# Kernel optimization log

Hardware: AMD Instinct MI355X
Metric: run time of the kernel (lower is better)

The kernel has to match this reference:

```python
import math
import jax, jax.numpy as jnp
import numpy as np

C = 32        # per-head dim
N_HEAD = 8
C_IN = 128

def setup_inputs() -> dict:
    key = jax.random.key(0)
    ks = jax.random.split(key, 10)
    B, S = 1, 256
    sc = 0.05  # keep logits in a sane range
    x    = jax.random.normal(ks[0], (B, S, S, C_IN), dtype=jnp.float32)
    bias = jax.random.normal(ks[1], (B, N_HEAD, S, S), dtype=jnp.float32)
    attention_mask = jax.random.randint(ks[2], (B, S, S), 0, 2).astype(bool)
    Wq = jax.random.normal(ks[3], (C_IN, C * N_HEAD), dtype=jnp.float32) * sc
    Wk = jax.random.normal(ks[4], (C_IN, C * N_HEAD), dtype=jnp.float32) * sc
    Wv = jax.random.normal(ks[5], (C_IN, C * N_HEAD), dtype=jnp.float32) * sc
    Wo = jax.random.normal(ks[6], (C * N_HEAD, C_IN), dtype=jnp.float32) * sc
    bo = jnp.zeros((C_IN,), dtype=jnp.float32)
    Wg = jax.random.normal(ks[7], (C_IN, C * N_HEAD), dtype=jnp.float32) * sc
    bg = jnp.zeros((C * N_HEAD,), dtype=jnp.float32)
    return {"x": x, "bias": bias, "attention_mask": attention_mask,
            "Wq": Wq, "Wk": Wk, "Wv": Wv, "Wo": Wo, "bo": bo, "Wg": Wg, "bg": bg}

def reference(x, bias, attention_mask, Wq, Wk, Wv, Wo, bo, Wg, bg):
    # x: [B, S, L, c_in]; attn_dim=2 is already the second-to-last dim,
    # so the torch movedim(attn_dim, -2) is the identity here.
    B, S, L, _ = x.shape
    q = x @ Wq  # [B, S, L, H*c]
    k = x @ Wk
    v = x @ Wv
    # split heads: [B, S, L, H, c] -> [B, S, H, L, c]
    def split_heads(t):
        return t.reshape(B, S, L, N_HEAD, C).transpose(0, 1, 3, 2, 4)
    q, k, v = split_heads(q), split_heads(k), split_heads(v)
    q = q / math.sqrt(C)
    # attention logits: [B, S, H, q, k]
    a = jnp.einsum('bshqc,bshkc->bshqk', q, k)
    # bias [B, H, q, k] -> broadcast over the axial batch dim S
    a = a + bias[:, None, :, :, :]
    # mask [B, S, k] -> [B, S, 1, 1, k]; masked positions get -inf
    m = attention_mask[:, :, None, None, :]
    a = jnp.where(m, a, -jnp.inf)
    a = jax.nn.softmax(a, axis=-1)
    o = jnp.einsum('bshqk,bshkc->bshqc', a, v)
    # merge heads: [B, S, H, L, c] -> [B, S, L, H*c]
    o = o.transpose(0, 1, 3, 2, 4).reshape(B, S, L, N_HEAD * C)
    # sigmoid gate
    g = jax.nn.sigmoid(x @ Wg + bg)
    o = g * o
    return o @ Wo + bo
```

## Files before the change

kernel.cpp:

```cpp
#include <hip/hip_runtime.h>
#include <hip/hip_bf16.h>
#include <cstdint>

#define CIN 128
#define NH 8
#define CH 32
#define LDQ16 1024

typedef short bf16x8 __attribute__((ext_vector_type(8)));
typedef short bf16x4 __attribute__((ext_vector_type(4)));
typedef float f32x4 __attribute__((ext_vector_type(4)));

__device__ __forceinline__ short f2bf(float f) {
  union { float f; unsigned u; } v; v.f = f;
  unsigned r = (v.u + 0x7FFFu + ((v.u >> 16) & 1u)) >> 16;
  return (short)r;
}
__device__ __forceinline__ float bf2f(short s) {
  union { unsigned u; float f; } v; v.u = ((unsigned)(unsigned short)s) << 16;
  return v.f;
}
__device__ __forceinline__ unsigned pk2bf(float a, float b) {
  union { __hip_bfloat162 h; unsigned u; } cv;
  cv.h = __float22bfloat162_rn(make_float2(a, b));
  return cv.u;
}

__global__ __launch_bounds__(256) void prep(
    const float* __restrict__ x,
    const float* __restrict__ Wq, const float* __restrict__ Wk,
    const float* __restrict__ Wv, const float* __restrict__ Wg,
    const float* __restrict__ Wo,
    const uint4* __restrict__ mask,
    short* __restrict__ xb, short* __restrict__ WT, short* __restrict__ WoT,
    unsigned int* __restrict__ flag)
{
  __shared__ int viol;
  const int b = blockIdx.x;
  if (b < 4096) {
    int base = (b * 256 + threadIdx.x) * 8;
    float4 a = *(const float4*)(x + base);
    float4 c = *(const float4*)(x + base + 4);
    bf16x8 r;
    r[0] = f2bf(a.x); r[1] = f2bf(a.y); r[2] = f2bf(a.z); r[3] = f2bf(a.w);
    r[4] = f2bf(c.x); r[5] = f2bf(c.y); r[6] = f2bf(c.z); r[7] = f2bf(c.w);
    *(bf16x8*)(xb + base) = r;
  } else if (b < 4160) {
    const float qscale = 0.17677669529663689f;
    int bb = b - 4096;
#pragma unroll
    for (int e = 0; e < 10; ++e) {
      int o = bb * 2560 + e * 256 + threadIdx.x;
      if (o < 131072) {
        int n = o >> 7, k = o & 127;
        int seg = n >> 8, nn = n & 255;
        const float* W = (seg == 0) ? Wq : (seg == 1) ? Wk : (seg == 2) ? Wv : Wg;
        float v = W[k * 256 + nn];
        if (seg == 0) v *= qscale;
        WT[o] = f2bf(v);
      } else {
        int o2 = o - 131072;
        int n = o2 >> 8, k = o2 & 255;
        WoT[o2] = f2bf(Wo[k * 128 + n]);
      }
    }
  } else {
    if (threadIdx.x == 0) viol = 0;
    __syncthreads();
    int v = 0;
#pragma unroll
    for (int j = 0; j < 16; ++j) {
      uint4 w = mask[j * 256 + threadIdx.x];
      v |= (w.x > 1u) | (w.y > 1u) | (w.z > 1u) | (w.w > 1u);
    }
    if (v) atomicOr(&viol, 1);
    __syncthreads();
    if (threadIdx.x == 0) *flag = viol ? 0u : 1u;
  }
}

__global__ __launch_bounds__(256) void proj_qkvg(
    const short* __restrict__ xb, const short* __restrict__ WT,
    const float* __restrict__ bg, short* __restrict__ qkvg)
{
  __shared__ short Al[64 * 136];
  __shared__ short Bl[128 * 136];
  const int tid = threadIdx.x;
  const int lane = tid & 63, w = tid >> 6;
  const int g = lane >> 4, c16 = lane & 15;
  const int wr = w & 1, wc = w >> 1;
  const int n0 = blockIdx.x * 128;
  const int row0 = blockIdx.y * 64;

  {
    const short* src = xb + (size_t)row0 * 128;
#pragma unroll
    for (int ch = 0; ch < 4; ++ch) {
      int c = ch * 256 + tid;
      int r = c >> 4, kc = c & 15;
      *(bf16x8*)&Al[r * 136 + kc * 8] = *(const bf16x8*)(src + r * 128 + kc * 8);
    }
    const short* wsrc = WT + (size_t)n0 * 128;
#pragma unroll
    for (int ch = 0; ch < 8; ++ch) {
      int c = ch * 256 + tid;
      int r = c >> 4, kc = c & 15;
      *(bf16x8*)&Bl[r * 136 + kc * 8] = *(const bf16x8*)(wsrc + r * 128 + kc * 8);
    }
  }
  __syncthreads();

  f32x4 acc[2][4];
#pragma unroll
  for (int rt = 0; rt < 2; ++rt)
#pragma unroll
    for (int ct = 0; ct < 4; ++ct) acc[rt][ct] = (f32x4){0.f, 0.f, 0.f, 0.f};

#pragma unroll
  for (int kk = 0; kk < 4; ++kk) {
    bf16x8 af[2], bfr[4];
#pragma unroll
    for (int rt = 0; rt < 2; ++rt)
      af[rt] = *(const bf16x8*)&Al[(wr * 32 + rt * 16 + c16) * 136 + kk * 32 + g * 8];
#pragma unroll
    for (int ct = 0; ct < 4; ++ct)
      bfr[ct] = *(const bf16x8*)&Bl[(wc * 64 + ct * 16 + c16) * 136 + kk * 32 + g * 8];
#pragma unroll
    for (int rt = 0; rt < 2; ++rt)
#pragma unroll
      for (int ct = 0; ct < 4; ++ct)
        acc[rt][ct] = __builtin_amdgcn_mfma_f32_16x16x32_bf16(af[rt], bfr[ct], acc[rt][ct], 0, 0, 0);
  }

  const int seg3 = (n0 >= 768);
  float bgv[4];
  if (seg3) {
#pragma unroll
    for (int ct = 0; ct < 4; ++ct)
      bgv[ct] = bg[n0 - 768 + wc * 64 + ct * 16 + c16];
  }
#pragma unroll
  for (int rt = 0; rt < 2; ++rt)
#pragma unroll
    for (int ct = 0; ct < 4; ++ct) {
      int col = n0 + wc * 64 + ct * 16 + c16;
#pragma unroll
      for (int i = 0; i < 4; ++i) {
        int row = row0 + wr * 32 + rt * 16 + g * 4 + i;
        float v = acc[rt][ct][i];
        if (seg3) v = 1.f / (1.f + __expf(-(v + bgv[ct])));
        qkvg[(size_t)row * LDQ16 + col] = f2bf(v);
      }
    }
}

__global__ __launch_bounds__(256, 4) void attn(
    short* __restrict__ qkvg, const float* __restrict__ bias,
    const void* __restrict__ maskraw, const unsigned int* __restrict__ flagp)
{
  __shared__ __align__(16) short lds16[19216];
  const int tid = threadIdx.x;
  const int h = blockIdx.x;
  const int srow = blockIdx.y;
  const int lane = tid & 63, w = tid >> 6;
  const int g = lane >> 4, c16 = lane & 15;
  short* rowbase = qkvg + (size_t)srow * (256 * LDQ16);
  unsigned int* vTd = (unsigned int*)&lds16[10240];
  float* lL = (float*)&lds16[18688];

  const unsigned int fl = *flagp;
  int mv = fl ? ((const int*)maskraw)[srow * 256 + tid]
              : (int)((const unsigned char*)maskraw)[srow * 256 + tid];
  unsigned long long bb = __ballot(mv != 0);
  unsigned int* scratch = (unsigned int*)&lds16[19200];
  if (lane == 0) {
    scratch[w * 2 + 0] = (unsigned int)bb;
    scratch[w * 2 + 1] = (unsigned int)(bb >> 32);
  }

#pragma unroll
  for (int it = 0; it < 2; ++it) {
    int c = it * 256 + tid;
    int kp = c >> 2, cv = c & 3;
    const short* p0 = rowbase + (size_t)(2 * kp) * LDQ16 + 256 + h * CH + cv * 8;
    bf16x8 k0 = *(const bf16x8*)p0;
    bf16x8 k1 = *(const bf16x8*)(p0 + LDQ16);
    bf16x8 v0 = *(const bf16x8*)(p0 + 256);
    bf16x8 v1 = *(const bf16x8*)(p0 + LDQ16 + 256);
    *(bf16x8*)&lds16[(2 * kp) * 40 + cv * 8] = k0;
    *(bf16x8*)&lds16[(2 * kp + 1) * 40 + cv * 8] = k1;
#pragma unroll
    for (int j = 0; j < 8; ++j)
      vTd[(cv * 8 + j) * 132 + kp] =
          ((unsigned)(unsigned short)v0[j]) | (((unsigned)(unsigned short)v1[j]) << 16);
  }

  const int qb = w * 64;
  bf16x8 qf[4];
#pragma unroll
  for (int qt = 0; qt < 4; ++qt)
    qf[qt] = *(const bf16x8*)(rowbase + (size_t)(qb + qt * 16 + c16) * LDQ16 + h * CH + g * 8);

  __syncthreads();

  unsigned int mb[8];
#pragma unroll
  for (int j = 0; j < 8; ++j) mb[j] = scratch[j];

  const f32x4 zero4 = {0.f, 0.f, 0.f, 0.f};
  float l_[4] = {0.f, 0.f, 0.f, 0.f};
  f32x4 O[4][2];
#pragma unroll
  for (int qt = 0; qt < 4; ++qt) { O[qt][0] = zero4; O[qt][1] = zero4; }

  const float* bh = bias + (size_t)h * 65536;

  for (int ch = 0; ch < 8; ++ch) {
    float4 bb4[2][4];
#pragma unroll
    for (int kt = 0; kt < 2; ++kt)
#pragma unroll
      for (int qt = 0; qt < 4; ++qt)
        bb4[kt][qt] = *(const float4*)(bh + (size_t)(qb + qt * 16 + c16) * 256 +
                                       ch * 32 + kt * 16 + g * 4);

#pragma unroll
    for (int kt = 0; kt < 2; ++kt) {
      bf16x8 kf = *(const bf16x8*)&lds16[(ch * 32 + kt * 16 + c16) * 40 + g * 8];
      bf16x4 vlo, vhi;
      {
        union { unsigned u[2]; bf16x4 v; } t0, t1;
        const unsigned* plo = &vTd[(size_t)c16 * 132 + ch * 16 + kt * 8 + g * 2];
        const unsigned* phi = &vTd[(size_t)(16 + c16) * 132 + ch * 16 + kt * 8 + g * 2];
        t0.u[0] = plo[0]; t0.u[1] = plo[1];
        t1.u[0] = phi[0]; t1.u[1] = phi[1];
        vlo = t0.v; vhi = t1.v;
      }
      const unsigned nib = (mb[ch] >> (kt * 16 + g * 4)) & 0xFu;
      float em[4];
#pragma unroll
      for (int i = 0; i < 4; ++i) em[i] = ((nib >> i) & 1u) ? 1.f : 0.f;
#pragma unroll
      for (int qt = 0; qt < 4; ++qt) {
        f32x4 S = __builtin_amdgcn_mfma_f32_16x16x32_bf16(kf, qf[qt], zero4, 0, 0, 0);
        float p0 = em[0] * __expf(fminf(S[0] + bb4[kt][qt].x, 85.f));
        float p1 = em[1] * __expf(fminf(S[1] + bb4[kt][qt].y, 85.f));
        float p2 = em[2] * __expf(fminf(S[2] + bb4[kt][qt].z, 85.f));
        float p3 = em[3] * __expf(fminf(S[3] + bb4[kt][qt].w, 85.f));
        l_[qt] += (p0 + p1) + (p2 + p3);
        union { unsigned u[2]; bf16x4 v; } pu;
        pu.u[0] = pk2bf(p0, p1);
        pu.u[1] = pk2bf(p2, p3);
        O[qt][0] = __builtin_amdgcn_mfma_f32_16x16x16bf16_1k(pu.v, vlo, O[qt][0], 0, 0, 0);
        O[qt][1] = __builtin_amdgcn_mfma_f32_16x16x16bf16_1k(pu.v, vhi, O[qt][1], 0, 0, 0);
      }
    }
  }

#pragma unroll
  for (int qt = 0; qt < 4; ++qt) {
    float v = l_[qt];
    v += __shfl_xor(v, 16);
    v += __shfl_xor(v, 32);
    if (lane < 16) lL[w * 64 + qt * 16 + c16] = v;
  }

#pragma unroll
  for (int qt = 0; qt < 4; ++qt)
#pragma unroll
    for (int i = 0; i < 4; ++i) {
      float l = lL[w * 64 + qt * 16 + g * 4 + i];
      float inv = 1.f / l;
      short* orow = rowbase + (size_t)(qb + qt * 16 + g * 4 + i) * LDQ16;
#pragma unroll
      for (int half = 0; half < 2; ++half) {
        int c = half * 16 + c16;
        float gv = bf2f(orow[768 + h * CH + c]);
        orow[h * CH + c] = f2bf(O[qt][half][i] * inv * gv);
      }
    }
}

__global__ __launch_bounds__(256) void out_proj(
    const short* __restrict__ og, const short* __restrict__ WoT,
    const float* __restrict__ bo, float* __restrict__ out)
{
  __shared__ short Al[64 * 136];
  __shared__ short Bl[128 * 136];
  const int tid = threadIdx.x;
  const int lane = tid & 63, w = tid >> 6;
  const int g = lane >> 4, c16 = lane & 15;
  const int wr = w & 1, wc = w >> 1;
  const int row0 = blockIdx.x * 64;

  f32x4 acc[2][4];
#pragma unroll
  for (int rt = 0; rt < 2; ++rt)
#pragma unroll
    for (int ct = 0; ct < 4; ++ct) acc[rt][ct] = (f32x4){0.f, 0.f, 0.f, 0.f};

  for (int kk0 = 0; kk0 < 256; kk0 += 128) {
#pragma unroll
    for (int ch = 0; ch < 4; ++ch) {
      int c = ch * 256 + tid;
      int r = c >> 4, kc = c & 15;
      *(bf16x8*)&Al[r * 136 + kc * 8] =
          *(const bf16x8*)(og + (size_t)(row0 + r) * LDQ16 + kk0 + kc * 8);
    }
#pragma unroll
    for (int ch = 0; ch < 8; ++ch) {
      int c = ch * 256 + tid;
      int r = c >> 4, kc = c & 15;
      *(bf16x8*)&Bl[r * 136 + kc * 8] =
          *(const bf16x8*)(WoT + (size_t)r * 256 + kk0 + kc * 8);
    }
    __syncthreads();
#pragma unroll
    for (int kk = 0; kk < 4; ++kk) {
      bf16x8 af[2], bfr[4];
#pragma unroll
      for (int rt = 0; rt < 2; ++rt)
        af[rt] = *(const bf16x8*)&Al[(wr * 32 + rt * 16 + c16) * 136 + kk * 32 + g * 8];
#pragma unroll
      for (int ct = 0; ct < 4; ++ct)
        bfr[ct] = *(const bf16x8*)&Bl[(wc * 64 + ct * 16 + c16) * 136 + kk * 32 + g * 8];
#pragma unroll
      for (int rt = 0; rt < 2; ++rt)
#pragma unroll
        for (int ct = 0; ct < 4; ++ct)
          acc[rt][ct] = __builtin_amdgcn_mfma_f32_16x16x32_bf16(af[rt], bfr[ct], acc[rt][ct], 0, 0, 0);
    }
    __syncthreads();
  }

#pragma unroll
  for (int rt = 0; rt < 2; ++rt)
#pragma unroll
    for (int ct = 0; ct < 4; ++ct) {
      int col = wc * 64 + ct * 16 + c16;
      float bv = bo[col];
#pragma unroll
      for (int i = 0; i < 4; ++i) {
        int row = row0 + wr * 32 + rt * 16 + g * 4 + i;
        out[(size_t)row * CIN + col] = acc[rt][ct][i] + bv;
      }
    }
}

extern "C" void kernel_launch(void* const* d_in, const int* in_sizes, int n_in,
                              void* d_out, int out_size, void* d_ws, size_t ws_size,
                              hipStream_t stream) {
  const float* x    = (const float*)d_in[0];
  const float* bias = (const float*)d_in[1];
  const void*  mask = d_in[2];
  const float* Wq   = (const float*)d_in[3];
  const float* Wk   = (const float*)d_in[4];
  const float* Wv   = (const float*)d_in[5];
  const float* Wo   = (const float*)d_in[6];
  const float* bo   = (const float*)d_in[7];
  const float* Wg   = (const float*)d_in[8];
  const float* bg   = (const float*)d_in[9];
  float* out = (float*)d_out;

  unsigned int* flag = (unsigned int*)d_ws;
  short* WT   = (short*)((char*)d_ws + 256);
  short* WoT  = WT + 131072;
  short* xb   = WoT + 32768;
  short* qkvg = xb + (size_t)65536 * 128;

  prep<<<4161, 256, 0, stream>>>(x, Wq, Wk, Wv, Wg, Wo, (const uint4*)mask,
                                 xb, WT, WoT, flag);
  proj_qkvg<<<dim3(8, 1024), 256, 0, stream>>>(xb, WT, bg, qkvg);
  attn<<<dim3(NH, 256), 256, 0, stream>>>(qkvg, bias, mask, flag);
  out_proj<<<1024, 256, 0, stream>>>(qkvg, WoT, bo, out);
}
```

Before: 259.8 us.

## Fuse QKVG projection, attention, gating and output projection into one kernel

Replaces the separate x-conversion, QKVG projection, attention and output-projection kernels with a single kernel per axial row (1024 threads). Each block converts x to bf16 in registers, projects Q/K/V/gate per head into LDS, runs the attention, applies the gate and accumulates the output projection. The aim is to remove the large global round trips of the bf16 x copy and the qkvg intermediate, plus several launches. In exchange there are only 256 large blocks with heavy LDS use, a serial head loop with barriers, and weight reads from global memory in every block.

After: 307.4 us. 18.3% more time.

```diff
diff --git a/kernel.cpp b/kernel.cpp
--- a/kernel.cpp
+++ b/kernel.cpp
@@ -5,7 +5,6 @@
 #define CIN 128
 #define NH 8
 #define CH 32
-#define LDQ16 1024
 
 typedef short bf16x8 __attribute__((ext_vector_type(8)));
 typedef short bf16x4 __attribute__((ext_vector_type(4)));
@@ -27,30 +26,20 @@
 }
 
 __global__ __launch_bounds__(256) void prep(
-    const float* __restrict__ x,
     const float* __restrict__ Wq, const float* __restrict__ Wk,
     const float* __restrict__ Wv, const float* __restrict__ Wg,
     const float* __restrict__ Wo,
     const uint4* __restrict__ mask,
-    short* __restrict__ xb, short* __restrict__ WT, short* __restrict__ WoT,
+    short* __restrict__ WT, short* __restrict__ WoT,
     unsigned int* __restrict__ flag)
 {
   __shared__ int viol;
   const int b = blockIdx.x;
-  if (b < 4096) {
-    int base = (b * 256 + threadIdx.x) * 8;
-    float4 a = *(const float4*)(x + base);
-    float4 c = *(const float4*)(x + base + 4);
-    bf16x8 r;
-    r[0] = f2bf(a.x); r[1] = f2bf(a.y); r[2] = f2bf(a.z); r[3] = f2bf(a.w);
-    r[4] = f2bf(c.x); r[5] = f2bf(c.y); r[6] = f2bf(c.z); r[7] = f2bf(c.w);
-    *(bf16x8*)(xb + base) = r;
-  } else if (b < 4160) {
+  if (b < 64) {
     const float qscale = 0.17677669529663689f;
-    int bb = b - 4096;
 #pragma unroll
     for (int e = 0; e < 10; ++e) {
-      int o = bb * 2560 + e * 256 + threadIdx.x;
+      int o = b * 2560 + e * 256 + threadIdx.x;
       if (o < 131072) {
         int n = o >> 7, k = o & 127;
         int seg = n >> 8, nn = n & 255;
@@ -79,272 +68,197 @@
   }
 }
 
-__global__ __launch_bounds__(256) void proj_qkvg(
-    const short* __restrict__ xb, const short* __restrict__ WT,
-    const float* __restrict__ bg, short* __restrict__ qkvg)
+__global__ __launch_bounds__(1024) void fused_attn(
+    const float* __restrict__ x, const short* __restrict__ WT,
+    const short* __restrict__ WoT,
+    const float* __restrict__ bias, const float* __restrict__ bg,
+    const float* __restrict__ bo,
+    const void* __restrict__ maskraw, const unsigned int* __restrict__ flagp,
+    float* __restrict__ out)
 {
-  __shared__ short Al[64 * 136];
-  __shared__ short Bl[128 * 136];
+  __shared__ __align__(16) short lds16[29456];
+  short* kL = lds16;
+  short* vL = &lds16[10240];
+  short* qL = &lds16[18688];
+  float* lL = (float*)&lds16[28928];
+  unsigned int* scratch = (unsigned int*)&lds16[29440];
+
   const int tid = threadIdx.x;
+  const int srow = blockIdx.x;
   const int lane = tid & 63, w = tid >> 6;
   const int g = lane >> 4, c16 = lane & 15;
-  const int wr = w & 1, wc = w >> 1;
-  const int n0 = blockIdx.x * 128;
-  const int row0 = blockIdx.y * 64;
-
+  const int myrow = w * 16;
+
+  const unsigned int fl = *flagp;
+  if (tid < 256) {
+    int mv = fl ? ((const int*)maskraw)[srow * 256 + tid]
+                : (int)((const unsigned char*)maskraw)[srow * 256 + tid];
+    unsigned long long bb = __ballot(mv != 0);
+    if (lane == 0) {
+      scratch[w * 2 + 0] = (unsigned int)bb;
+      scratch[w * 2 + 1] = (unsigned int)(bb >> 32);
+    }
+  }
+
+  bf16x8 xf[4];
   {
-    const short* src = xb + (size_t)row0 * 128;
-#pragma unroll
-    for (int ch = 0; ch < 4; ++ch) {
-      int c = ch * 256 + tid;
-      int r = c >> 4, kc = c & 15;
-      *(bf16x8*)&Al[r * 136 + kc * 8] = *(const bf16x8*)(src + r * 128 + kc * 8);
-    }
-    const short* wsrc = WT + (size_t)n0 * 128;
-#pragma unroll
+    const float* xs = x + ((size_t)srow * 256 + myrow + c16) * 128 + g * 8;
+#pragma unroll
+    for (int kk = 0; kk < 4; ++kk) {
+      float4 a = *(const float4*)(xs + kk * 32);
+      float4 b = *(const float4*)(xs + kk * 32 + 4);
+      union { unsigned u[4]; bf16x8 v; } p;
+      p.u[0] = pk2bf(a.x, a.y); p.u[1] = pk2bf(a.z, a.w);
+      p.u[2] = pk2bf(b.x, b.y); p.u[3] = pk2bf(b.z, b.w);
+      xf[kk] = p.v;
+    }
+  }
+
+  __syncthreads();
+
+  unsigned int mb[8];
+#pragma unroll
+  for (int j = 0; j < 8; ++j)
+    mb[j] = (unsigned int)__builtin_amdgcn_readfirstlane((int)scratch[j]);
+
+  const f32x4 zero4 = {0.f, 0.f, 0.f, 0.f};
+  f32x4 acc_out[8];
+#pragma unroll
+  for (int ct = 0; ct < 8; ++ct) acc_out[ct] = zero4;
+
+#pragma unroll 1
+  for (int h = 0; h < 8; ++h) {
+    f32x4 ga0, ga1;
+    {
+      f32x4 a0 = zero4, a1 = zero4;
+#pragma unroll
+      for (int kk = 0; kk < 4; ++kk) {
+        bf16x8 w0 = *(const bf16x8*)(WT + (size_t)(256 + h * CH + c16) * 128 + kk * 32 + g * 8);
+        bf16x8 w1 = *(const bf16x8*)(WT + (size_t)(256 + h * CH + 16 + c16) * 128 + kk * 32 + g * 8);
+        a0 = __builtin_amdgcn_mfma_f32_16x16x32_bf16(w0, xf[kk], a0, 0, 0, 0);
+        a1 = __builtin_amdgcn_mfma_f32_16x16x32_bf16(w1, xf[kk], a1, 0, 0, 0);
+      }
+      union { unsigned u[2]; bf16x4 v; } p0, p1;
+      p0.u[0] = pk2bf(a0[0], a0[1]); p0.u[1] = pk2bf(a0[2], a0[3]);
+      p1.u[0] = pk2bf(a1[0], a1[1]); p1.u[1] = pk2bf(a1[2], a1[3]);
+      *(bf16x4*)&kL[(myrow + c16) * 40 + g * 4]      = p0.v;
+      *(bf16x4*)&kL[(myrow + c16) * 40 + 16 + g * 4] = p1.v;
+    }
+    {
+      f32x4 a0 = zero4, a1 = zero4;
+#pragma unroll
+      for (int kk = 0; kk < 4; ++kk) {
+        bf16x8 w0 = *(const bf16x8*)(WT + (size_t)(h * CH + c16) * 128 + kk * 32 + g * 8);
+        bf16x8 w1 = *(const bf16x8*)(WT + (size_t)(h * CH + 16 + c16) * 128 + kk * 32 + g * 8);
+        a0 = __builtin_amdgcn_mfma_f32_16x16x32_bf16(w0, xf[kk], a0, 0, 0, 0);
+        a1 = __builtin_amdgcn_mfma_f32_16x16x32_bf16(w1, xf[kk], a1, 0, 0, 0);
+      }
+      union { unsigned u[2]; bf16x4 v; } p0, p1;
+      p0.u[0] = pk2bf(a0[0], a0[1]); p0.u[1] = pk2bf(a0[2], a0[3]);
+      p1.u[0] = pk2bf(a1[0], a1[1]); p1.u[1] = pk2bf(a1[2], a1[3]);
+      *(bf16x4*)&qL[(myrow + c16) * 40 + g * 4]      = p0.v;
+      *(bf16x4*)&qL[(myrow + c16) * 40 + 16 + g * 4] = p1.v;
+    }
+    {
+      f32x4 a0 = zero4, a1 = zero4;
+#pragma unroll
+      for (int kk = 0; kk < 4; ++kk) {
+        bf16x8 w0 = *(const bf16x8*)(WT + (size_t)(512 + h * CH + c16) * 128 + kk * 32 + g * 8);
+        bf16x8 w1 = *(const bf16x8*)(WT + (size_t)(512 + h * CH + 16 + c16) * 128 + kk * 32 + g * 8);
+        a0 = __builtin_amdgcn_mfma_f32_16x16x32_bf16(xf[kk], w0, a0, 0, 0, 0);
+        a1 = __builtin_amdgcn_mfma_f32_16x16x32_bf16(xf[kk], w1, a1, 0, 0, 0);
+      }
+      union { unsigned u[2]; bf16x4 v; } p0, p1;
+      p0.u[0] = pk2bf(a0[0], a0[1]); p0.u[1] = pk2bf(a0[2], a0[3]);
+      p1.u[0] = pk2bf(a1[0], a1[1]); p1.u[1] = pk2bf(a1[2], a1[3]);
+      *(bf16x4*)&vL[(size_t)c16 * 264 + myrow + g * 4]        = p0.v;
+      *(bf16x4*)&vL[(size_t)(16 + c16) * 264 + myrow + g * 4] = p1.v;
+    }
+    {
+      f32x4 a0 = zero4, a1 = zero4;
+#pragma unroll
+      for (int kk = 0; kk < 4; ++kk) {
+        bf16x8 w0 = *(const bf16x8*)(WT + (size_t)(768 + h * CH + c16) * 128 + kk * 32 + g * 8);
+        bf16x8 w1 = *(const bf16x8*)(WT + (size_t)(768 + h * CH + 16 + c16) * 128 + kk * 32 + g * 8);
+        a0 = __builtin_amdgcn_mfma_f32_16x16x32_bf16(xf[kk], w0, a0, 0, 0, 0);
+        a1 = __builtin_amdgcn_mfma_f32_16x16x32_bf16(xf[kk], w1, a1, 0, 0, 0);
+      }
+      ga0 = a0; ga1 = a1;
+    }
+    __syncthreads();
+
+    bf16x8 qf = *(const bf16x8*)&qL[(myrow + c16) * 40 + g * 8];
+    float l_ = 0.f;
+    f32x4 O0 = zero4, O1 = zero4;
+    const float* bh = bias + (size_t)h * 65536;
+
+#pragma unroll 1
     for (int ch = 0; ch < 8; ++ch) {
-      int c = ch * 256 + tid;
-      int r = c >> 4, kc = c & 15;
-      *(bf16x8*)&Bl[r * 136 + kc * 8] = *(const bf16x8*)(wsrc + r * 128 + kc * 8);
-    }
-  }
-  __syncthreads();
-
-  f32x4 acc[2][4];
-#pragma unroll
-  for (int rt = 0; rt < 2; ++rt)
-#pragma unroll
-    for (int ct = 0; ct < 4; ++ct) acc[rt][ct] = (f32x4){0.f, 0.f, 0.f, 0.f};
-
-#pragma unroll
-  for (int kk = 0; kk < 4; ++kk) {
-    bf16x8 af[2], bfr[4];
-#pragma unroll
-    for (int rt = 0; rt < 2; ++rt)
-      af[rt] = *(const bf16x8*)&Al[(wr * 32 + rt * 16 + c16) * 136 + kk * 32 + g * 8];
-#pragma unroll
-    for (int ct = 0; ct < 4; ++ct)
-      bfr[ct] = *(const bf16x8*)&Bl[(wc * 64 + ct * 16 + c16) * 136 + kk * 32 + g * 8];
-#pragma unroll
-    for (int rt = 0; rt < 2; ++rt)
-#pragma unroll
-      for (int ct = 0; ct < 4; ++ct)
-        acc[rt][ct] = __builtin_amdgcn_mfma_f32_16x16x32_bf16(af[rt], bfr[ct], acc[rt][ct], 0, 0, 0);
-  }
-
-  const int seg3 = (n0 >= 768);
-  float bgv[4];
-  if (seg3) {
-#pragma unroll
-    for (int ct = 0; ct < 4; ++ct)
-      bgv[ct] = bg[n0 - 768 + wc * 64 + ct * 16 + c16];
-  }
-#pragma unroll
-  for (int rt = 0; rt < 2; ++rt)
-#pragma unroll
-    for (int ct = 0; ct < 4; ++ct) {
-      int col = n0 + wc * 64 + ct * 16 + c16;
-#pragma unroll
-      for (int i = 0; i < 4; ++i) {
-        int row = row0 + wr * 32 + rt * 16 + g * 4 + i;
-        float v = acc[rt][ct][i];
-        if (seg3) v = 1.f / (1.f + __expf(-(v + bgv[ct])));
-        qkvg[(size_t)row * LDQ16 + col] = f2bf(v);
-      }
-    }
-}
-
-__global__ __launch_bounds__(256, 4) void attn(
-    short* __restrict__ qkvg, const float* __restrict__ bias,
-    const void* __restrict__ maskraw, const unsigned int* __restrict__ flagp)
-{
-  __shared__ __align__(16) short lds16[19216];
-  const int tid = threadIdx.x;
-  const int h = blockIdx.x;
-  const int srow = blockIdx.y;
-  const int lane = tid & 63, w = tid >> 6;
-  const int g = lane >> 4, c16 = lane & 15;
-  short* rowbase = qkvg + (size_t)srow * (256 * LDQ16);
-  unsigned int* vTd = (unsigned int*)&lds16[10240];
-  float* lL = (float*)&lds16[18688];
-
-  const unsigned int fl = *flagp;
-  int mv = fl ? ((const int*)maskraw)[srow * 256 + tid]
-              : (int)((const unsigned char*)maskraw)[srow * 256 + tid];
-  unsigned long long bb = __ballot(mv != 0);
-  unsigned int* scratch = (unsigned int*)&lds16[19200];
-  if (lane == 0) {
-    scratch[w * 2 + 0] = (unsigned int)bb;
-    scratch[w * 2 + 1] = (unsigned int)(bb >> 32);
-  }
-
-#pragma unroll
-  for (int it = 0; it < 2; ++it) {
-    int c = it * 256 + tid;
-    int kp = c >> 2, cv = c & 3;
-    const short* p0 = rowbase + (size_t)(2 * kp) * LDQ16 + 256 + h * CH + cv * 8;
-    bf16x8 k0 = *(const bf16x8*)p0;
-    bf16x8 k1 = *(const bf16x8*)(p0 + LDQ16);
-    bf16x8 v0 = *(const bf16x8*)(p0 + 256);
-    bf16x8 v1 = *(const bf16x8*)(p0 + LDQ16 + 256);
-    *(bf16x8*)&lds16[(2 * kp) * 40 + cv * 8] = k0;
-    *(bf16x8*)&lds16[(2 * kp + 1) * 40 + cv * 8] = k1;
-#pragma unroll
-    for (int j = 0; j < 8; ++j)
-      vTd[(cv * 8 + j) * 132 + kp] =
-          ((unsigned)(unsigned short)v0[j]) | (((unsigned)(unsigned short)v1[j]) << 16);
-  }
-
-  const int qb = w * 64;
-  bf16x8 qf[4];
-#pragma unroll
-  for (int qt = 0; qt < 4; ++qt)
-    qf[qt] = *(const bf16x8*)(rowbase + (size_t)(qb + qt * 16 + c16) * LDQ16 + h * CH + g * 8);
-
-  __syncthreads();
-
-  unsigned int mb[8];
-#pragma unroll
-  for (int j = 0; j < 8; ++j) mb[j] = scratch[j];
-
-  const f32x4 zero4 = {0.f, 0.f, 0.f, 0.f};
-  float l_[4] = {0.f, 0.f, 0.f, 0.f};
-  f32x4 O[4][2];
-#pragma unroll
-  for (int qt = 0; qt < 4; ++qt) { O[qt][0] = zero4; O[qt][1] = zero4; }
-
-  const float* bh = bias + (size_t)h * 65536;
-
-  for (int ch = 0; ch < 8; ++ch) {
-    float4 bb4[2][4];
-#pragma unroll
-    for (int kt = 0; kt < 2; ++kt)
-#pragma unroll
-      for (int qt = 0; qt < 4; ++qt)
-        bb4[kt][qt] = *(const float4*)(bh + (size_t)(qb + qt * 16 + c16) * 256 +
-                                       ch * 32 + kt * 16 + g * 4);
-
-#pragma unroll
-    for (int kt = 0; kt < 2; ++kt) {
-      bf16x8 kf = *(const bf16x8*)&lds16[(ch * 32 + kt * 16 + c16) * 40 + g * 8];
-      bf16x4 vlo, vhi;
-      {
-        union { unsigned u[2]; bf16x4 v; } t0, t1;
-        const unsigned* plo = &vTd[(size_t)c16 * 132 + ch * 16 + kt * 8 + g * 2];
-        const unsigned* phi = &vTd[(size_t)(16 + c16) * 132 + ch * 16 + kt * 8 + g * 2];
-        t0.u[0] = plo[0]; t0.u[1] = plo[1];
-        t1.u[0] = phi[0]; t1.u[1] = phi[1];
-        vlo = t0.v; vhi = t1.v;
-      }
-      const unsigned nib = (mb[ch] >> (kt * 16 + g * 4)) & 0xFu;
-      float em[4];
-#pragma unroll
-      for (int i = 0; i < 4; ++i) em[i] = ((nib >> i) & 1u) ? 1.f : 0.f;
-#pragma unroll
-      for (int qt = 0; qt < 4; ++qt) {
-        f32x4 S = __builtin_amdgcn_mfma_f32_16x16x32_bf16(kf, qf[qt], zero4, 0, 0, 0);
-        float p0 = em[0] * __expf(fminf(S[0] + bb4[kt][qt].x, 85.f));
-        float p1 = em[1] * __expf(fminf(S[1] + bb4[kt][qt].y, 85.f));
-        float p2 = em[2] * __expf(fminf(S[2] + bb4[kt][qt].z, 85.f));
-        float p3 = em[3] * __expf(fminf(S[3] + bb4[kt][qt].w, 85.f));
-        l_[qt] += (p0 + p1) + (p2 + p3);
+      float4 bb0 = *(const float4*)(bh + (size_t)(myrow + c16) * 256 + ch * 32 + g * 4);
+      float4 bb1 = *(const float4*)(bh + (size_t)(myrow + c16) * 256 + ch * 32 + 16 + g * 4);
+#pragma unroll
+      for (int kt = 0; kt < 2; ++kt) {
+        bf16x8 kf = *(const bf16x8*)&kL[(ch * 32 + kt * 16 + c16) * 40 + g * 8];
+        bf16x4 vlo = *(const bf16x4*)&vL[(size_t)c16 * 264 + ch * 32 + kt * 16 + g * 4];
+        bf16x4 vhi = *(const bf16x4*)&vL[(size_t)(16 + c16) * 264 + ch * 32 + kt * 16 + g * 4];
+        const unsigned nib = (mb[ch] >> (kt * 16 + g * 4)) & 0xFu;
+        float em0 = (nib & 1u) ? 1.f : 0.f;
+        float em1 = (nib & 2u) ? 1.f : 0.f;
+        float em2 = (nib & 4u) ? 1.f : 0.f;
+        float em3 = (nib & 8u) ? 1.f : 0.f;
+        const float4 bb = kt ? bb1 : bb0;
+        f32x4 S = __builtin_amdgcn_mfma_f32_16x16x32_bf16(kf, qf, zero4, 0, 0, 0);
+        float p0 = em0 * __expf(fminf(S[0] + bb.x, 85.f));
+        float p1 = em1 * __expf(fminf(S[1] + bb.y, 85.f));
+        float p2 = em2 * __expf(fminf(S[2] + bb.z, 85.f));
+        float p3 = em3 * __expf(fminf(S[3] + bb.w, 85.f));
+        l_ += (p0 + p1) + (p2 + p3);
         union { unsigned u[2]; bf16x4 v; } pu;
         pu.u[0] = pk2bf(p0, p1);
         pu.u[1] = pk2bf(p2, p3);
-        O[qt][0] = __builtin_amdgcn_mfma_f32_16x16x16bf16_1k(pu.v, vlo, O[qt][0], 0, 0, 0);
-        O[qt][1] = __builtin_amdgcn_mfma_f32_16x16x16bf16_1k(pu.v, vhi, O[qt][1], 0, 0, 0);
-      }
-    }
-  }
-
-#pragma unroll
-  for (int qt = 0; qt < 4; ++qt) {
-    float v = l_[qt];
-    v += __shfl_xor(v, 16);
-    v += __shfl_xor(v, 32);
-    if (lane < 16) lL[w * 64 + qt * 16 + c16] = v;
-  }
-
-#pragma unroll
-  for (int qt = 0; qt < 4; ++qt)
-#pragma unroll
-    for (int i = 0; i < 4; ++i) {
-      float l = lL[w * 64 + qt * 16 + g * 4 + i];
-      float inv = 1.f / l;
-      short* orow = rowbase + (size_t)(qb + qt * 16 + g * 4 + i) * LDQ16;
-#pragma unroll
-      for (int half = 0; half < 2; ++half) {
-        int c = half * 16 + c16;
-        float gv = bf2f(orow[768 + h * CH + c]);
-        orow[h * CH + c] = f2bf(O[qt][half][i] * inv * gv);
-      }
-    }
-}
-
-__global__ __launch_bounds__(256) void out_proj(
-    const short* __restrict__ og, const short* __restrict__ WoT,
-    const float* __restrict__ bo, float* __restrict__ out)
-{
-  __shared__ short Al[64 * 136];
-  __shared__ short Bl[128 * 136];
-  const int tid = threadIdx.x;
-  const int lane = tid & 63, w = tid >> 6;
-  const int g = lane >> 4, c16 = lane & 15;
-  const int wr = w & 1, wc = w >> 1;
-  const int row0 = blockIdx.x * 64;
-
-  f32x4 acc[2][4];
-#pragma unroll
-  for (int rt = 0; rt < 2; ++rt)
-#pragma unroll
-    for (int ct = 0; ct < 4; ++ct) acc[rt][ct] = (f32x4){0.f, 0.f, 0.f, 0.f};
-
-  for (int kk0 = 0; kk0 < 256; kk0 += 128) {
-#pragma unroll
-    for (int ch = 0; ch < 4; ++ch) {
-      int c = ch * 256 + tid;
-      int r = c >> 4, kc = c & 15;
-      *(bf16x8*)&Al[r * 136 + kc * 8] =
-          *(const bf16x8*)(og + (size_t)(row0 + r) * LDQ16 + kk0 + kc * 8);
-    }
-#pragma unroll
-    for (int ch = 0; ch < 8; ++ch) {
-      int c = ch * 256 + tid;
-      int r = c >> 4, kc = c & 15;
-      *(bf16x8*)&Bl[r * 136 + kc * 8] =
-          *(const bf16x8*)(WoT + (size_t)r * 256 + kk0 + kc * 8);
-    }
-    __syncthreads();
-#pragma unroll
-    for (int kk = 0; kk < 4; ++kk) {
-      bf16x8 af[2], bfr[4];
-#pragma unroll
-      for (int rt = 0; rt < 2; ++rt)
-        af[rt] = *(const bf16x8*)&Al[(wr * 32 + rt * 16 + c16) * 136 + kk * 32 + g * 8];
-#pragma unroll
-      for (int ct = 0; ct < 4; ++ct)
-        bfr[ct] = *(const bf16x8*)&Bl[(wc * 64 + ct * 16 + c16) * 136 + kk * 32 + g * 8];
-#pragma unroll
-      for (int rt = 0; rt < 2; ++rt)
-#pragma unroll
-        for (int ct = 0; ct < 4; ++ct)
-          acc[rt][ct] = __builtin_amdgcn_mfma_f32_16x16x32_bf16(af[rt], bfr[ct], acc[rt][ct], 0, 0, 0);
-    }
-    __syncthreads();
-  }
-
-#pragma unroll
-  for (int rt = 0; rt < 2; ++rt)
-#pragma unroll
-    for (int ct = 0; ct < 4; ++ct) {
-      int col = wc * 64 + ct * 16 + c16;
-      float bv = bo[col];
+        O0 = __builtin_amdgcn_mfma_f32_16x16x16bf16_1k(pu.v, vlo, O0, 0, 0, 0);
+        O1 = __builtin_amdgcn_mfma_f32_16x16x16bf16_1k(pu.v, vhi, O1, 0, 0, 0);
+      }
+    }
+
+    {
+      float v = l_;
+      v += __shfl_xor(v, 16);
+      v += __shfl_xor(v, 32);
+      if (lane < 16) lL[myrow + c16] = v;
+    }
+
+    {
+      float bgl0 = bg[h * CH + c16];
+      float bgl1 = bg[h * CH + 16 + c16];
 #pragma unroll
       for (int i = 0; i < 4; ++i) {
-        int row = row0 + wr * 32 + rt * 16 + g * 4 + i;
-        out[(size_t)row * CIN + col] = acc[rt][ct][i] + bv;
-      }
-    }
+        float inv = 1.f / lL[myrow + g * 4 + i];
+        float g0 = 1.f / (1.f + __expf(-(ga0[i] + bgl0)));
+        float g1 = 1.f / (1.f + __expf(-(ga1[i] + bgl1)));
+        qL[(myrow + g * 4 + i) * 40 + c16]      = f2bf(O0[i] * inv * g0);
+        qL[(myrow + g * 4 + i) * 40 + 16 + c16] = f2bf(O1[i] * inv * g1);
+      }
+    }
+
+    {
+      bf16x8 of = *(const bf16x8*)&qL[(myrow + c16) * 40 + g * 8];
+#pragma unroll
+      for (int ct = 0; ct < 8; ++ct) {
+        bf16x8 wo = *(const bf16x8*)(WoT + (size_t)(ct * 16 + c16) * 256 + h * 32 + g * 8);
+        acc_out[ct] = __builtin_amdgcn_mfma_f32_16x16x32_bf16(of, wo, acc_out[ct], 0, 0, 0);
+      }
+    }
+    __syncthreads();
+  }
+
+#pragma unroll
+  for (int ct = 0; ct < 8; ++ct) {
+    float bv = bo[ct * 16 + c16];
+#pragma unroll
+    for (int i = 0; i < 4; ++i)
+      out[((size_t)srow * 256 + myrow + g * 4 + i) * 128 + ct * 16 + c16] = acc_out[ct][i] + bv;
+  }
 }
 
 extern "C" void kernel_launch(void* const* d_in, const int* in_sizes, int n_in,
@@ -363,14 +277,11 @@
   float* out = (float*)d_out;
 
   unsigned int* flag = (unsigned int*)d_ws;
-  short* WT   = (short*)((char*)d_ws + 256);
-  short* WoT  = WT + 131072;
-  short* xb   = WoT + 32768;
-  short* qkvg = xb + (size_t)65536 * 128;
-
-  prep<<<4161, 256, 0, stream>>>(x, Wq, Wk, Wv, Wg, Wo, (const uint4*)mask,
-                                 xb, WT, WoT, flag);
-  proj_qkvg<<<dim3(8, 1024), 256, 0, stream>>>(xb, WT, bg, qkvg);
-  attn<<<dim3(NH, 256), 256, 0, stream>>>(qkvg, bias, mask, flag);
-  out_proj<<<1024, 256, 0, stream>>>(qkvg, WoT, bo, out);
-}
+  short* WT  = (short*)((char*)d_ws + 256);
+  short* WoT = WT + 131072;
+
+  prep<<<65, 256, 0, stream>>>(Wq, Wk, Wv, Wg, Wo, (const uint4*)mask,
+                               WT, WoT, flag);
+  fused_attn<<<256, 1024, 0, stream>>>(x, WT, WoT, bias, bg, bo,
+                                       mask, flag, out);
+}
```
